# Optimization experiments

Hardware: AMD Instinct MI355X
Metric: run time of the kernel (lower is better)

The kernel has to match this reference:

```python
import jax, jax.numpy as jnp
import numpy as np

B, S, E, H = 8, 1024, 1024, 16
EPS = 1e-3  # tf.keras LayerNormalization default epsilon


def setup_inputs() -> dict:
    key = jax.random.key(0)
    ks = jax.random.split(key, 5)
    x = jax.random.normal(ks[0], (B, S, E), dtype=jnp.float32)
    Wq = jax.random.normal(ks[1], (E, E), dtype=jnp.float32) * 0.02
    Wk = jax.random.normal(ks[2], (E, E), dtype=jnp.float32) * 0.02
    Wv = jax.random.normal(ks[3], (E, E), dtype=jnp.float32) * 0.02
    # original init is zeros; use small random values so the bias path is exercised
    rel_table = jax.random.normal(ks[4], (2 * S - 1, H), dtype=jnp.float32) * 0.02
    gamma = jnp.ones((E,), dtype=jnp.float32)
    beta = jnp.zeros((E,), dtype=jnp.float32)
    return {"x": x, "Wq": Wq, "Wk": Wk, "Wv": Wv, "rel_table": rel_table,
            "gamma": gamma, "beta": beta}


def reference(x, Wq, Wk, Wv, rel_table, gamma, beta):
    b, s, e = x.shape
    h = rel_table.shape[1]
    scale = e ** (-0.5)  # NOTE: scales by full emb_size, not head_dim (faithful)

    def split_heads(t):  # (b, s, e) -> (b, h, s, d)
        return t.reshape(b, s, h, -1).transpose(0, 2, 1, 3)

    q = split_heads(x @ Wq)
    k = split_heads(x @ Wk)
    v = split_heads(x @ Wv)

    attn = jnp.einsum("bhqd,bhkd->bhqk", q, k) * scale
    attn = jax.nn.softmax(attn, axis=-1)

    # relative bias: gather then the exact (quirky) reshape sequence of the original
    r = jnp.arange(s)
    rel_index = jnp.clip(r[None, :] - r[:, None] + (s - 1), 0, 2 * s - 2)  # (s, s)
    bias = rel_table[rel_index]              # (s, s, h)
    bias = bias.reshape(-1).reshape(h, s, s)  # faithful flat-order reinterpretation
    attn = attn + bias[None]  # added POST-softmax, as in the original

    out = jnp.einsum("bhqk,bhkd->bhqd", attn, v)
    out = out.transpose(0, 2, 1, 3).reshape(b, s, e)

    # LayerNorm over last axis
    mu = jnp.mean(out, axis=-1, keepdims=True)
    var = jnp.var(out, axis=-1, keepdims=True)
    out = (out - mu) / jnp.sqrt(var + EPS) * gamma + beta
    return out
```

## Files before the change

kernel.cpp:

```cpp
#include <hip/hip_runtime.h>
#include <hip/hip_bf16.h>

#define PB 8
#define PS 1024
#define PE 1024
#define PH 16
#define PD 64
#define EPSLN 1e-3f
#define SCALE 0.03125f

typedef __attribute__((ext_vector_type(8))) short bf16x8;
typedef __attribute__((ext_vector_type(4))) float f32x4;
typedef __attribute__((ext_vector_type(16))) float f32x16;

__device__ __forceinline__ unsigned short f2bf(float f) {
    unsigned int u = __float_as_uint(f);
    u += 0x7FFFu + ((u >> 16) & 1u);
    return (unsigned short)(u >> 16);
}

__device__ __forceinline__ void gload_lds16(const void* g, void* l) {
    __builtin_amdgcn_global_load_lds(
        (const __attribute__((address_space(1))) unsigned int*)g,
        (__attribute__((address_space(3))) unsigned int*)l,
        16, 0, 0);
}

__device__ __forceinline__ unsigned int cvtpk_bf16(float lo, float hi) {
    unsigned int r;
    asm("v_cvt_pk_bf16_f32 %0, %1, %2" : "=v"(r) : "v"(lo), "v"(hi));
    return r;
}

__device__ __forceinline__ void plswap(unsigned int& a, unsigned int& b) {
    asm("v_permlane32_swap_b32 %0, %1" : "+v"(a), "+v"(b));
}

__global__ __launch_bounds__(256) void conv_x(
    const float* __restrict__ X, unsigned short* __restrict__ Xb)
{
    const size_t i = (size_t)blockIdx.x * 256 + threadIdx.x;
    const float4* p = reinterpret_cast<const float4*>(X) + i * 2;
    float4 a = p[0], b = p[1];
    unsigned short r[8];
    r[0] = f2bf(a.x); r[1] = f2bf(a.y); r[2] = f2bf(a.z); r[3] = f2bf(a.w);
    r[4] = f2bf(b.x); r[5] = f2bf(b.y); r[6] = f2bf(b.z); r[7] = f2bf(b.w);
    *reinterpret_cast<uint4*>(Xb + i * 8) = *reinterpret_cast<const uint4*>(r);
}

__global__ __launch_bounds__(256) void conv_w(
    const float* __restrict__ Wq, const float* __restrict__ Wk,
    const float* __restrict__ Wv, unsigned short* __restrict__ Wtb)
{
    const int proj = blockIdx.z;
    const float* W = (proj == 0) ? Wq : (proj == 1) ? Wk : Wv;
    __shared__ float tile[32][33];
    const int n0 = blockIdx.x * 32, k0 = blockIdx.y * 32;
    const int tx = threadIdx.x & 31, ty = threadIdx.x >> 5;
#pragma unroll
    for (int i = 0; i < 4; ++i)
        tile[ty + i * 8][tx] = W[(size_t)(k0 + ty + i * 8) * PE + n0 + tx];
    __syncthreads();
#pragma unroll
    for (int i = 0; i < 4; ++i)
        Wtb[(size_t)(proj * 1024 + n0 + ty + i * 8) * 1024 + k0 + tx] =
            f2bf(tile[tx][ty + i * 8]);
}

__global__ __launch_bounds__(256) void conv_rel(
    const float* __restrict__ rel, unsigned short* __restrict__ relbf)
{
    const int i = blockIdx.x * 1024 + threadIdx.x * 4;
#pragma unroll
    for (int k = 0; k < 4; ++k)
        if (i + k < (2 * PS - 1) * PH) relbf[i + k] = f2bf(rel[i + k]);
}

__global__ __launch_bounds__(256) void qkv_mfma(
    const unsigned short* __restrict__ Xb,
    const unsigned short* __restrict__ Wtb,
    unsigned short* __restrict__ QKV)
{
    const int orig = blockIdx.x;
    const int wg = (orig & 7) * 192 + (orig >> 3);
    const int nblk = wg % 24, mblk = wg / 24;
    const int m0 = mblk * 128, n0 = nblk * 128;

    __shared__ __align__(16) unsigned short As[128 * 64];
    __shared__ __align__(16) unsigned short Bs[128 * 64];

    const int t = threadIdx.x;
    const int w = t >> 6, l = t & 63;
    const int lane15 = l & 15, lhi = l >> 4;
    const int wm = w >> 1, wn = w & 1;

    f32x4 acc[4][4] = {};

    for (int k0 = 0; k0 < 1024; k0 += 64) {
        __syncthreads();
#pragma unroll
        for (int c = 0; c < 4; ++c) {
            const int ci = (w * 4 + c) * 64 + l;
            const int r = ci >> 3;
            const int srccl = (ci & 7) ^ (r & 7);
            gload_lds16(Xb  + (size_t)(m0 + r) * 1024 + k0 + srccl * 8, &As[ci * 8]);
            gload_lds16(Wtb + (size_t)(n0 + r) * 1024 + k0 + srccl * 8, &Bs[ci * 8]);
        }
        __syncthreads();
#pragma unroll
        for (int kk = 0; kk < 2; ++kk) {
            bf16x8 af[4], bf[4];
#pragma unroll
            for (int mi = 0; mi < 4; ++mi) {
                const int row = wm * 64 + mi * 16 + lane15;
                af[mi] = *reinterpret_cast<const bf16x8*>(
                    &As[row * 64 + (((kk * 4 + lhi) ^ (row & 7)) << 3)]);
            }
#pragma unroll
            for (int ni = 0; ni < 4; ++ni) {
                const int row = wn * 64 + ni * 16 + lane15;
                bf[ni] = *reinterpret_cast<const bf16x8*>(
                    &Bs[row * 64 + (((kk * 4 + lhi) ^ (row & 7)) << 3)]);
            }
#pragma unroll
            for (int mi = 0; mi < 4; ++mi)
#pragma unroll
                for (int ni = 0; ni < 4; ++ni)
                    acc[mi][ni] = __builtin_amdgcn_mfma_f32_16x16x32_bf16(
                        af[mi], bf[ni], acc[mi][ni], 0, 0, 0);
        }
    }
#pragma unroll
    for (int mi = 0; mi < 4; ++mi)
#pragma unroll
        for (int ni = 0; ni < 4; ++ni)
#pragma unroll
            for (int r = 0; r < 4; ++r) {
                const int gr = m0 + wm * 64 + mi * 16 + lhi * 4 + r;
                const int gc = n0 + wn * 64 + ni * 16 + lane15;
                QKV[(size_t)gr * 3072 + gc] = f2bf(acc[mi][ni][r]);
            }
}

__global__ __launch_bounds__(256) void vtrans(
    const unsigned short* __restrict__ QKV, unsigned short* __restrict__ VT)
{
    const int j0 = blockIdx.x * 64, b = blockIdx.y, h = blockIdx.z;
    __shared__ unsigned short tile[64][72];
    const int t = threadIdx.x;

#pragma unroll
    for (int it = 0; it < 2; ++it) {
        const int jr = it * 32 + (t >> 3), dc = t & 7;
        uint4 d = *reinterpret_cast<const uint4*>(
            QKV + ((size_t)(b * PS + j0 + jr)) * 3072 + 2048 + h * 64 + dc * 8);
        *reinterpret_cast<uint4*>(&tile[jr][dc * 8]) = d;
    }
    __syncthreads();
    const int d = t & 63, jc = t >> 6;
    unsigned short out[16];
#pragma unroll
    for (int k = 0; k < 16; ++k) out[k] = tile[jc * 16 + k][d];
    unsigned short* dst = VT + ((size_t)((h * 8 + b) * 64 + d)) * 1024 + j0 + jc * 16;
    *reinterpret_cast<uint4*>(dst)     = *reinterpret_cast<const uint4*>(out);
    *reinterpret_cast<uint4*>(dst + 8) = *reinterpret_cast<const uint4*>(out + 8);
}

__global__ __launch_bounds__(256) void attn_mfma(
    const unsigned short* __restrict__ qkv,
    const unsigned short* __restrict__ VT,
    const unsigned short* __restrict__ relbf,
    float* __restrict__ O)
{
    __shared__ __align__(16) unsigned short Ks[2][64 * 64];
    __shared__ __align__(16) unsigned short Vt[2][64 * 64];
    __shared__ float Pl[4][32];

    const int orig = blockIdx.x;
    const int wg = (orig & 7) * 128 + (orig >> 3);
    const int qt = wg & 7;
    const int h  = (wg >> 3) & 15;
    const int b  = wg >> 7;

    const int t = threadIdx.x;
    const int w = t >> 6, l = t & 63;
    const int lane31 = l & 31, hi = l >> 5;

    const int qrow_g = qt * 128 + w * 32 + lane31;

    bf16x8 qf[4];
    {
        const unsigned short* qp =
            qkv + ((size_t)(b * PS) + qrow_g) * 3072 + h * 64 + hi * 8;
#pragma unroll
        for (int dw = 0; dw < 4; ++dw)
            qf[dw] = *reinterpret_cast<const bf16x8*>(qp + dw * 16);
    }

    const unsigned short* Kg = qkv + (size_t)(b * PS) * 3072 + 1024 + h * 64;
    const unsigned short* Vg = VT + ((size_t)((h * 8 + b) * 64)) * 1024;

    const int s1 = (h << 6) | (qrow_g >> 4);
    const int s2hi = (qrow_g & 15) << 6;

    f32x16 accP[2] = {};
    f32x16 accB[2] = {};
    float lsum = 0.f;

#define ATTN_STAGE(buf, j0)                                                          \
    {                                                                                \
        _Pragma("unroll")                                                            \
        for (int it = 0; it < 2; ++it) {                                             \
            const int ci = it * 256 + t;                                             \
            const int r = ci >> 3;                                                   \
            const int scl = (ci & 7) ^ (r & 7);                                      \
            gload_lds16(Kg + (size_t)((j0) + r) * 3072 + scl * 8, &Ks[buf][ci * 8]); \
            gload_lds16(Vg + (size_t)r * 1024 + (j0) + scl * 8, &Vt[buf][ci * 8]);   \
        }                                                                            \
    }

    ATTN_STAGE(0, 0)

    for (int tt = 0; tt < 16; ++tt) {
        const int cur = tt & 1;
        const int j0 = tt * 64;

        bf16x8 af[4];
        __builtin_amdgcn_sched_barrier(0);
#pragma unroll
        for (int jw = 0; jw < 4; ++jw) {
            const int ridx = (s2hi | ((j0 >> 4) + jw)) - s1 + (PS - 1);
            af[jw] = *reinterpret_cast<const bf16x8*>(relbf + ridx * PH + hi * 8);
        }
        __builtin_amdgcn_sched_barrier(0);
        if (tt < 15) {
            ATTN_STAGE(cur ^ 1, j0 + 64)
            __builtin_amdgcn_sched_barrier(0);
            asm volatile("s_waitcnt vmcnt(8)" ::: "memory");
        } else {
            asm volatile("s_waitcnt vmcnt(4)" ::: "memory");
        }
        __builtin_amdgcn_sched_barrier(0);
        __builtin_amdgcn_s_barrier();
        __builtin_amdgcn_sched_barrier(0);

        bf16x8 pfrag[4];
#pragma unroll
        for (int jt = 0; jt < 2; ++jt) {
            f32x16 sc = {};
#pragma unroll
            for (int dw = 0; dw < 4; ++dw) {
                const int row = jt * 32 + lane31;
                bf16x8 aK = *reinterpret_cast<const bf16x8*>(
                    &Ks[cur][row * 64 + (((dw * 2 + hi) ^ (row & 7)) << 3)]);
                sc = __builtin_amdgcn_mfma_f32_32x32x16_bf16(aK, qf[dw], sc, 0, 0, 0);
            }
            float p[16];
#pragma unroll
            for (int r = 0; r < 16; ++r) {
                p[r] = __expf(sc[r] * SCALE);
                lsum += p[r];
            }
            unsigned int a0 = cvtpk_bf16(p[0],  p[1]),  a1 = cvtpk_bf16(p[2],  p[3]);
            unsigned int b0 = cvtpk_bf16(p[4],  p[5]),  b1 = cvtpk_bf16(p[6],  p[7]);
            unsigned int c0 = cvtpk_bf16(p[8],  p[9]),  c1 = cvtpk_bf16(p[10], p[11]);
            unsigned int d0 = cvtpk_bf16(p[12], p[13]), d1 = cvtpk_bf16(p[14], p[15]);
            plswap(a0, b0); plswap(a1, b1);
            plswap(c0, d0); plswap(c1, d1);
            union { unsigned int u[4]; bf16x8 v; } pk0, pk1;
            pk0.u[0] = a0; pk0.u[1] = a1; pk0.u[2] = b0; pk0.u[3] = b1;
            pk1.u[0] = c0; pk1.u[1] = c1; pk1.u[2] = d0; pk1.u[3] = d1;
            pfrag[jt * 2]     = pk0.v;
            pfrag[jt * 2 + 1] = pk1.v;
        }

#pragma unroll
        for (int jw = 0; jw < 4; ++jw) {
#pragma unroll
            for (int dt = 0; dt < 2; ++dt) {
                const int row = dt * 32 + lane31;
                bf16x8 bV = *reinterpret_cast<const bf16x8*>(
                    &Vt[cur][row * 64 + (((jw * 2 + hi) ^ (row & 7)) << 3)]);
                accP[dt] = __builtin_amdgcn_mfma_f32_32x32x16_bf16(
                    pfrag[jw], bV, accP[dt], 0, 0, 0);
                accB[dt] = __builtin_amdgcn_mfma_f32_32x32x16_bf16(
                    af[jw], bV, accB[dt], 0, 0, 0);
            }
        }
        __builtin_amdgcn_s_barrier();
    }
#undef ATTN_STAGE

    const float ltot = lsum + __shfl_xor(lsum, 32);
    if (l < 32) Pl[w][l] = 1.0f / ltot;
    __syncthreads();

#pragma unroll
    for (int dt = 0; dt < 2; ++dt)
#pragma unroll
        for (int r = 0; r < 16; ++r) {
            const int rl = (r & 3) + 8 * (r >> 2) + 4 * hi;
            const float invl = Pl[w][rl];
            O[((size_t)(b * PS + qt * 128 + w * 32 + rl)) * PE + h * 64 + dt * 32 + lane31]
                = accP[dt][r] * invl + accB[dt][r];
        }
}

__global__ __launch_bounds__(256) void layernorm_inplace(
    float* __restrict__ O,
    const float* __restrict__ gamma,
    const float* __restrict__ beta)
{
    const int row = blockIdx.x;
    float* p = O + (size_t)row * PE;
    const int t = threadIdx.x;

    float4 x = reinterpret_cast<float4*>(p)[t];
    float s  = x.x + x.y + x.z + x.w;
    float s2 = x.x * x.x + x.y * x.y + x.z * x.z + x.w * x.w;

#pragma unroll
    for (int off = 1; off < 64; off <<= 1) {
        s  += __shfl_xor(s, off, 64);
        s2 += __shfl_xor(s2, off, 64);
    }
    __shared__ float red[2][4];
    const int wid = t >> 6;
    if ((t & 63) == 0) { red[0][wid] = s; red[1][wid] = s2; }
    __syncthreads();
    const float ts  = red[0][0] + red[0][1] + red[0][2] + red[0][3];
    const float ts2 = red[1][0] + red[1][1] + red[1][2] + red[1][3];

    const float mu  = ts * (1.f / PE);
    const float var = ts2 * (1.f / PE) - mu * mu;
    const float inv = rsqrtf(var + EPSLN);

    const float4 g  = reinterpret_cast<const float4*>(gamma)[t];
    const float4 bb = reinterpret_cast<const float4*>(beta)[t];
    float4 y;
    y.x = (x.x - mu) * inv * g.x + bb.x;
    y.y = (x.y - mu) * inv * g.y + bb.y;
    y.z = (x.z - mu) * inv * g.z + bb.z;
    y.w = (x.w - mu) * inv * g.w + bb.w;
    reinterpret_cast<float4*>(p)[t] = y;
}

extern "C" void kernel_launch(void* const* d_in, const int* in_sizes, int n_in,
                              void* d_out, int out_size, void* d_ws, size_t ws_size,
                              hipStream_t stream) {
    (void)in_sizes; (void)n_in; (void)out_size; (void)ws_size;
    const float* x     = (const float*)d_in[0];
    const float* Wq    = (const float*)d_in[1];
    const float* Wk    = (const float*)d_in[2];
    const float* Wv    = (const float*)d_in[3];
    const float* rel   = (const float*)d_in[4];
    const float* gamma = (const float*)d_in[5];
    const float* beta  = (const float*)d_in[6];
    float* out = (float*)d_out;

    char* ws = (char*)d_ws;
    unsigned short* Xb    = (unsigned short*)ws;
    unsigned short* Wtb   = (unsigned short*)(ws + 16777216);
    unsigned short* QKV   = (unsigned short*)(ws + 23068672);
    unsigned short* VT    = (unsigned short*)(ws + 73400320);
    unsigned short* relbf = (unsigned short*)ws;

    conv_x<<<4096, 256, 0, stream>>>(x, Xb);
    conv_w<<<dim3(32, 32, 3), 256, 0, stream>>>(Wq, Wk, Wv, Wtb);
    qkv_mfma<<<1536, 256, 0, stream>>>(Xb, Wtb, QKV);
    conv_rel<<<32, 256, 0, stream>>>(rel, relbf);
    vtrans<<<dim3(16, 8, 16), 256, 0, stream>>>(QKV, VT);
    attn_mfma<<<1024, 256, 0, stream>>>(QKV, VT, relbf, out);
    layernorm_inplace<<<PB * PS, 256, 0, stream>>>(out, gamma, beta);
}
```

Measured before the change: 175.6 us.

## Compute softmax row sums via MFMA with ones, widen LDS swizzle, add setprio

Replaces the per-lane VALU accumulation of exp values and the LDS-based row-sum exchange with an extra MFMA that multiplies the bf16 P fragments by a ones vector, so the softmax denominator comes out in the output layout. It also widens the LDS XOR swizzle to include row bits 3-4, which is meant to reduce bank conflicts. The relative-bias pointer is precomputed outside the loop, and s_setprio is raised around the MFMA blocks. In exchange it adds MFMA work and sums the bf16-rounded P values instead of the fp32 ones, which slightly changes numerics.

```diff
diff --git a/kernel.cpp b/kernel.cpp
--- a/kernel.cpp
+++ b/kernel.cpp
@@ -36,6 +36,8 @@
     asm("v_permlane32_swap_b32 %0, %1" : "+v"(a), "+v"(b));
 }
 
+#define SWZF(row, chunk) (((chunk) ^ ((row) & 7) ^ (((row) >> 3) & 3)))
+
 __global__ __launch_bounds__(256) void conv_x(
     const float* __restrict__ X, unsigned short* __restrict__ Xb)
 {
@@ -174,7 +176,6 @@
 {
     __shared__ __align__(16) unsigned short Ks[2][64 * 64];
     __shared__ __align__(16) unsigned short Vt[2][64 * 64];
-    __shared__ float Pl[4][32];
 
     const int orig = blockIdx.x;
     const int wg = (orig & 7) * 128 + (orig >> 3);
@@ -202,10 +203,14 @@
 
     const int s1 = (h << 6) | (qrow_g >> 4);
     const int s2hi = (qrow_g & 15) << 6;
+    const unsigned short* relp = relbf + (size_t)(s2hi - s1 + PS - 1) * PH + hi * 8;
 
     f32x16 accP[2] = {};
     f32x16 accB[2] = {};
-    float lsum = 0.f;
+    f32x16 accL = {};
+    bf16x8 ones;
+#pragma unroll
+    for (int i = 0; i < 8; ++i) ones[i] = (short)0x3F80;
 
 #define ATTN_STAGE(buf, j0)                                                          \
     {                                                                                \
@@ -213,7 +218,7 @@
         for (int it = 0; it < 2; ++it) {                                             \
             const int ci = it * 256 + t;                                             \
             const int r = ci >> 3;                                                   \
-            const int scl = (ci & 7) ^ (r & 7);                                      \
+            const int scl = SWZF(r, ci & 7);                                         \
             gload_lds16(Kg + (size_t)((j0) + r) * 3072 + scl * 8, &Ks[buf][ci * 8]); \
             gload_lds16(Vg + (size_t)r * 1024 + (j0) + scl * 8, &Vt[buf][ci * 8]);   \
         }                                                                            \
@@ -228,10 +233,8 @@
         bf16x8 af[4];
         __builtin_amdgcn_sched_barrier(0);
 #pragma unroll
-        for (int jw = 0; jw < 4; ++jw) {
-            const int ridx = (s2hi | ((j0 >> 4) + jw)) - s1 + (PS - 1);
-            af[jw] = *reinterpret_cast<const bf16x8*>(relbf + ridx * PH + hi * 8);
-        }
+        for (int jw = 0; jw < 4; ++jw)
+            af[jw] = *reinterpret_cast<const bf16x8*>(relp + j0 + jw * 16);
         __builtin_amdgcn_sched_barrier(0);
         if (tt < 15) {
             ATTN_STAGE(cur ^ 1, j0 + 64)
@@ -248,19 +251,18 @@
 #pragma unroll
         for (int jt = 0; jt < 2; ++jt) {
             f32x16 sc = {};
+            __builtin_amdgcn_s_setprio(1);
 #pragma unroll
             for (int dw = 0; dw < 4; ++dw) {
                 const int row = jt * 32 + lane31;
                 bf16x8 aK = *reinterpret_cast<const bf16x8*>(
-                    &Ks[cur][row * 64 + (((dw * 2 + hi) ^ (row & 7)) << 3)]);
+                    &Ks[cur][row * 64 + (SWZF(row, dw * 2 + hi) << 3)]);
                 sc = __builtin_amdgcn_mfma_f32_32x32x16_bf16(aK, qf[dw], sc, 0, 0, 0);
             }
+            __builtin_amdgcn_s_setprio(0);
             float p[16];
 #pragma unroll
-            for (int r = 0; r < 16; ++r) {
-                p[r] = __expf(sc[r] * SCALE);
-                lsum += p[r];
-            }
+            for (int r = 0; r < 16; ++r) p[r] = __expf(sc[r] * SCALE);
             unsigned int a0 = cvtpk_bf16(p[0],  p[1]),  a1 = cvtpk_bf16(p[2],  p[3]);
             unsigned int b0 = cvtpk_bf16(p[4],  p[5]),  b1 = cvtpk_bf16(p[6],  p[7]);
             unsigned int c0 = cvtpk_bf16(p[8],  p[9]),  c1 = cvtpk_bf16(p[10], p[11]);
@@ -274,35 +276,33 @@
             pfrag[jt * 2 + 1] = pk1.v;
         }
 
+        __builtin_amdgcn_s_setprio(1);
 #pragma unroll
         for (int jw = 0; jw < 4; ++jw) {
+            accL = __builtin_amdgcn_mfma_f32_32x32x16_bf16(pfrag[jw], ones, accL, 0, 0, 0);
 #pragma unroll
             for (int dt = 0; dt < 2; ++dt) {
                 const int row = dt * 32 + lane31;
                 bf16x8 bV = *reinterpret_cast<const bf16x8*>(
-                    &Vt[cur][row * 64 + (((jw * 2 + hi) ^ (row & 7)) << 3)]);
+                    &Vt[cur][row * 64 + (SWZF(row, jw * 2 + hi) << 3)]);
                 accP[dt] = __builtin_amdgcn_mfma_f32_32x32x16_bf16(
                     pfrag[jw], bV, accP[dt], 0, 0, 0);
                 accB[dt] = __builtin_amdgcn_mfma_f32_32x32x16_bf16(
                     af[jw], bV, accB[dt], 0, 0, 0);
             }
         }
+        __builtin_amdgcn_s_setprio(0);
         __builtin_amdgcn_s_barrier();
     }
 #undef ATTN_STAGE
-
-    const float ltot = lsum + __shfl_xor(lsum, 32);
-    if (l < 32) Pl[w][l] = 1.0f / ltot;
-    __syncthreads();
 
 #pragma unroll
     for (int dt = 0; dt < 2; ++dt)
 #pragma unroll
         for (int r = 0; r < 16; ++r) {
             const int rl = (r & 3) + 8 * (r >> 2) + 4 * hi;
-            const float invl = Pl[w][rl];
             O[((size_t)(b * PS + qt * 128 + w * 32 + rl)) * PE + h * 64 + dt * 32 + lane31]
-                = accP[dt][r] * invl + accB[dt][r];
+                = accP[dt][r] / accL[r] + accB[dt][r];
         }
 }
 
```

After: 171.3 us. 1.03x faster.
